# Kernel optimization log

Hardware: AMD Instinct MI355X
Metric: run time of the kernel (lower is better)

The kernel has to match this reference:

```python
import math
import jax, jax.numpy as jnp
import numpy as np

B, S, D, H = 1, 4096, 1024, 16
HD = D // H


def setup_inputs() -> dict:
    key = jax.random.key(0)
    ks = jax.random.split(key, 11)
    s = 0.02
    inp = {
        "q": jax.random.normal(ks[0], (B, S, D), jnp.float32),
        "k": jax.random.normal(ks[1], (B, S, D), jnp.float32),
        "v": jax.random.normal(ks[2], (B, S, D), jnp.float32),
        # causal boolean mask, broadcastable over [B, H, S, S]
        "mask": jnp.tril(jnp.ones((S, S), jnp.bool_))[None, None],
        "Wq": jax.random.normal(ks[3], (D, D), jnp.float32) * s,
        "bq": jnp.zeros((D,), jnp.float32),
        "Wk": jax.random.normal(ks[4], (D, D), jnp.float32) * s,
        "bk": jnp.zeros((D,), jnp.float32),
        "Wv": jax.random.normal(ks[5], (D, D), jnp.float32) * s,
        "bv": jnp.zeros((D,), jnp.float32),
        "Wo": jax.random.normal(ks[6], (D, D), jnp.float32) * s,
        "bo": jnp.zeros((D,), jnp.float32),
    }
    return inp


def reference(q, k, v, mask, Wq, bq, Wk, bk, Wv, bv, Wo, bo):
    # projections (torch Linear: x @ W.T + b; here W is stored already transposed)
    qp = (q @ Wq + bq).reshape(B, S, H, HD)
    kp = (k @ Wk + bk).reshape(B, S, H, HD)
    vp = (v @ Wv + bv).reshape(B, S, H, HD)
    # scores: [B, H, S, S]
    scores = jnp.einsum("bqhd,bkhd->bhqk", qp, kp) / math.sqrt(HD)
    scores = jnp.where(mask, scores, -jnp.inf)
    attn = jax.nn.softmax(scores, axis=-1)
    # context: [B, H, S, HD] -> [B, S, D]
    ctx = jnp.einsum("bhqk,bkhd->bqhd", attn, vp).reshape(B, S, D)
    return ctx @ Wo + bo
```

## Files before the change

### kernel.cpp

```cpp
#include <hip/hip_runtime.h>
#include <hip/hip_bf16.h>


#define S_LEN 4096
#define D_DIM 1024
#define NHEAD 16
#define HDIM  64

typedef __hip_bfloat16 bf16;
typedef __attribute__((ext_vector_type(8))) short bf16x8v;
typedef __attribute__((ext_vector_type(4))) float f32x4;

#define MFMA16(a, b, c) __builtin_amdgcn_mfma_f32_16x16x32_bf16((a), (b), (c), 0, 0, 0)

__device__ __forceinline__ void async_cp16(const void* g, void* l) {
    __builtin_amdgcn_global_load_lds(
        (const __attribute__((address_space(1))) unsigned int*)g,
        (__attribute__((address_space(3))) unsigned int*)l, 16, 0, 0);
}

__global__ __launch_bounds__(256) void cvt_bf16_k(
    const float* __restrict__ x0, const float* __restrict__ x1,
    const float* __restrict__ x2,
    bf16* __restrict__ y0, bf16* __restrict__ y1, bf16* __restrict__ y2)
{
    const float* x = (blockIdx.z == 0) ? x0 : (blockIdx.z == 1) ? x1 : x2;
    bf16*       y = (blockIdx.z == 0) ? y0 : (blockIdx.z == 1) ? y1 : y2;
    const size_t i = ((size_t)blockIdx.x * 256 + threadIdx.x);
    const float4 v = ((const float4*)x)[i];
    union { bf16 h[4]; short4 s; } u;
    u.h[0] = __float2bfloat16(v.x);
    u.h[1] = __float2bfloat16(v.y);
    u.h[2] = __float2bfloat16(v.z);
    u.h[3] = __float2bfloat16(v.w);
    ((short4*)y)[i] = u.s;
}

__global__ __launch_bounds__(256) void transpose_cvt_k(
    const float* __restrict__ W0, const float* __restrict__ W1,
    const float* __restrict__ W2, const float* __restrict__ W3,
    bf16* __restrict__ T0, bf16* __restrict__ T1,
    bf16* __restrict__ T2, bf16* __restrict__ T3)
{
    const float* W = (blockIdx.z == 0) ? W0 : (blockIdx.z == 1) ? W1
                   : (blockIdx.z == 2) ? W2 : W3;
    bf16*       Wt = (blockIdx.z == 0) ? T0 : (blockIdx.z == 1) ? T1
                   : (blockIdx.z == 2) ? T2 : T3;
    __shared__ float t[32][33];
    const int bx = blockIdx.x << 5, by = blockIdx.y << 5;
    const int tx = threadIdx.x & 31, ty = threadIdx.x >> 5;
#pragma unroll
    for (int i = 0; i < 32; i += 8)
        t[ty + i][tx] = W[(size_t)(by + ty + i) * D_DIM + bx + tx];
    __syncthreads();
#pragma unroll
    for (int i = 0; i < 32; i += 8)
        Wt[(size_t)(bx + ty + i) * D_DIM + by + tx] = __float2bfloat16(t[tx][ty + i]);
}

struct GemmJob {
    const bf16* A; const bf16* Wt; const float* bias; void* out;
    int mode; float scale;
};

__global__ __launch_bounds__(256) void gemm_k(GemmJob j0, GemmJob j1, GemmJob j2)
{
    const GemmJob j = (blockIdx.z == 0) ? j0 : (blockIdx.z == 1) ? j1 : j2;
    const int K = D_DIM;
    const int bn = blockIdx.x << 6;
    const int bm = blockIdx.y << 7;
    const int tid = threadIdx.x;
    const int w = tid >> 6, lane = tid & 63;
    const int col = lane & 15, g = lane >> 4;
    const int wr = (w >> 1) << 6, wc = (w & 1) << 5;

    __shared__ bf16 As[128 * 64];
    __shared__ bf16 Bs[64 * 64];

    f32x4 acc[4][2];
#pragma unroll
    for (int i = 0; i < 4; ++i)
#pragma unroll
        for (int jj = 0; jj < 2; ++jj) acc[i][jj] = (f32x4){0.f, 0.f, 0.f, 0.f};

    for (int kb = 0; kb < K; kb += 64) {
        __syncthreads();
#pragma unroll
        for (int e = 0; e < 4; ++e) {
            const int lin = (e << 8) + tid;
            const int row = lin >> 3, kc = lin & 7;
            async_cp16(j.A + (size_t)(bm + row) * K + kb + (kc << 3), &As[lin << 3]);
        }
#pragma unroll
        for (int e = 0; e < 2; ++e) {
            const int lin = (e << 8) + tid;
            const int row = lin >> 3, kc = lin & 7;
            async_cp16(j.Wt + (size_t)(bn + row) * K + kb + (kc << 3), &Bs[lin << 3]);
        }
        __syncthreads();

#pragma unroll
        for (int s = 0; s < 2; ++s) {
            bf16x8v af[4], bfv[2];
#pragma unroll
            for (int i = 0; i < 4; ++i)
                af[i] = *(const bf16x8v*)&As[((wr + (i << 4) + col) << 6) + (s << 5) + (g << 3)];
#pragma unroll
            for (int jj = 0; jj < 2; ++jj)
                bfv[jj] = *(const bf16x8v*)&Bs[((wc + (jj << 4) + col) << 6) + (s << 5) + (g << 3)];
#pragma unroll
            for (int i = 0; i < 4; ++i)
#pragma unroll
                for (int jj = 0; jj < 2; ++jj)
                    acc[i][jj] = MFMA16(af[i], bfv[jj], acc[i][jj]);
        }
    }

#pragma unroll
    for (int i = 0; i < 4; ++i)
#pragma unroll
    for (int jj = 0; jj < 2; ++jj)
#pragma unroll
    for (int reg = 0; reg < 4; ++reg) {
        const int row = bm + wr + (i << 4) + (g << 2) + reg;
        const int cg  = bn + wc + (jj << 4) + col;
        const float vv = (acc[i][jj][reg] + j.bias[cg]) * j.scale;
        if (j.mode == 0)
            ((bf16*)j.out)[(((size_t)(cg >> 6)) * S_LEN + row) * HDIM + (cg & 63)] =
                __float2bfloat16(vv);
        else if (j.mode == 2)
            ((bf16*)j.out)[((size_t)(cg >> 6) * HDIM + (cg & 63)) * S_LEN + row] =
                __float2bfloat16(vv);
        else
            ((float*)j.out)[(size_t)row * D_DIM + cg] = vv;
    }
}

__global__ __launch_bounds__(256) void attn_mfma_k(
    const bf16* __restrict__ Qp, const bf16* __restrict__ Kp,
    const bf16* __restrict__ Vt, bf16* __restrict__ ctx)
{
    __shared__ bf16 Ks[4096];
    __shared__ bf16 Vs[4096];
    __shared__ bf16 Ps[4][1024];

    const int bid = blockIdx.x;
    const int qb  = 63 - (bid >> 4);
    const int h   = bid & 15;
    const int q0  = qb << 6;
    const int tid = threadIdx.x, w = tid >> 6, lane = tid & 63;
    const int col = lane & 15, g = lane >> 4;

    const bf16* Kh = Kp + (size_t)h * S_LEN * HDIM;
    const bf16* Vh = Vt + (size_t)h * HDIM * S_LEN;

    const size_t qrow_base = ((size_t)h * S_LEN + q0 + (w << 4) + col) * HDIM + (g << 3);
    const bf16x8v qf0 = *(const bf16x8v*)(Qp + qrow_base);
    const bf16x8v qf1 = *(const bf16x8v*)(Qp + qrow_base + 32);

    const int sig_r = (col >> 2) | (((col & 3) ^ (g & 1)) << 2);
    const int pr0 = (((g) << 4) | sig_r) << 3;
    const int pr1 = (((4 + g) << 4) | sig_r) << 3;
    int pw[4][4];
#pragma unroll
    for (int t = 0; t < 4; ++t) {
        const int Gw = (t << 1) + (col >> 3);
#pragma unroll
        for (int reg = 0; reg < 4; ++reg) {
            const int sig = g | (((reg ^ (Gw & 1)) & 3) << 2);
            pw[t][reg] = (((Gw << 4) | sig) << 3) + (col & 7);
        }
    }

    float pl[4] = {0.f, 0.f, 0.f, 0.f};
    f32x4 acco[4];
#pragma unroll
    for (int t = 0; t < 4; ++t) acco[t] = (f32x4){0.f, 0.f, 0.f, 0.f};

    const int nkb = qb + 1;
    for (int kb = 0; kb < nkb; ++kb) {
        const int kk0 = kb << 6;
        __syncthreads();
#pragma unroll
        for (int e = 0; e < 2; ++e) {
            const int lin = (e << 8) + tid;
            const int t = lin >> 7, G = (lin >> 4) & 7, c = lin & 15;
            async_cp16(Kh + (size_t)(kk0 + (t << 4) + c) * HDIM + (G << 3),
                       &Ks[lin << 3]);
            async_cp16(Vh + (size_t)((t << 4) + c) * S_LEN + kk0 + (G << 3),
                       &Vs[lin << 3]);
        }
        __syncthreads();

        f32x4 sa[4];
#pragma unroll
        for (int t = 0; t < 4; ++t) sa[t] = (f32x4){0.f, 0.f, 0.f, 0.f};
#pragma unroll
        for (int t = 0; t < 4; ++t) {
            sa[t] = MFMA16(qf0, *(const bf16x8v*)&Ks[((t << 7) + (g << 4) + col) << 3], sa[t]);
            sa[t] = MFMA16(qf1, *(const bf16x8v*)&Ks[((t << 7) + 64 + (g << 4) + col) << 3], sa[t]);
        }

        const bool lastt = (kb == nkb - 1);
#pragma unroll
        for (int t = 0; t < 4; ++t) {
#pragma unroll
            for (int reg = 0; reg < 4; ++reg) {
                float p;
                if (lastt && (kk0 + (t << 4) + col > q0 + (w << 4) + (g << 2) + reg))
                    p = 0.f;
                else
                    p = __expf(sa[t][reg]);
                pl[reg] += p;
                Ps[w][pw[t][reg]] = __float2bfloat16(p);
            }
        }

        const bf16x8v pf0 = *(const bf16x8v*)&Ps[w][pr0];
        const bf16x8v pf1 = *(const bf16x8v*)&Ps[w][pr1];
#pragma unroll
        for (int t = 0; t < 4; ++t) {
            acco[t] = MFMA16(pf0, *(const bf16x8v*)&Vs[((t << 7) + (g << 4) + col) << 3], acco[t]);
            acco[t] = MFMA16(pf1, *(const bf16x8v*)&Vs[((t << 7) + 64 + (g << 4) + col) << 3], acco[t]);
        }
    }

    float lrow[4];
#pragma unroll
    for (int reg = 0; reg < 4; ++reg) {
        float l = pl[reg];
        l += __shfl_xor(l, 1);
        l += __shfl_xor(l, 2);
        l += __shfl_xor(l, 4);
        l += __shfl_xor(l, 8);
        lrow[reg] = l;
    }

#pragma unroll
    for (int t = 0; t < 4; ++t)
#pragma unroll
        for (int reg = 0; reg < 4; ++reg) {
            const int row = q0 + (w << 4) + (g << 2) + reg;
            ctx[(size_t)row * D_DIM + h * HDIM + (t << 4) + col] =
                __float2bfloat16(acco[t][reg] / lrow[reg]);
        }
}

extern "C" void kernel_launch(void* const* d_in, const int* in_sizes, int n_in,
                              void* d_out, int out_size, void* d_ws, size_t ws_size,
                              hipStream_t stream)
{
    const float* q  = (const float*)d_in[0];
    const float* k  = (const float*)d_in[1];
    const float* v  = (const float*)d_in[2];
    const float* Wq = (const float*)d_in[4];
    const float* bq = (const float*)d_in[5];
    const float* Wk = (const float*)d_in[6];
    const float* bk = (const float*)d_in[7];
    const float* Wv = (const float*)d_in[8];
    const float* bv = (const float*)d_in[9];
    const float* Wo = (const float*)d_in[10];
    const float* bo = (const float*)d_in[11];

    const size_t PE  = (size_t)S_LEN * D_DIM;
    const size_t WTE = (size_t)D_DIM * D_DIM;

    const dim3 tg(32, 32, 4);
    const dim3 gg(D_DIM / 64, S_LEN / 128, 1);
    const dim3 gg3(D_DIM / 64, S_LEN / 128, 3);
    const dim3 cg((unsigned)(PE / 1024), 1, 3);

    if (ws_size >= (size_t)64 * 1024 * 1024) {
        bf16* Qb = (bf16*)d_ws;
        bf16* Kb = Qb + PE;
        bf16* Vb = Kb + PE;
        bf16* Qp = Vb + PE;
        bf16* Kp = Qp + PE;
        bf16* Vt = Kp + PE;
        bf16* Wtq = Vt + PE;
        bf16* Wtk = Wtq + WTE;
        bf16* Wtv = Wtk + WTE;
        bf16* Wto = Wtv + WTE;
        bf16* ctx = Qb;

        transpose_cvt_k<<<tg, 256, 0, stream>>>(Wq, Wk, Wv, Wo, Wtq, Wtk, Wtv, Wto);
        cvt_bf16_k<<<cg, 256, 0, stream>>>(q, k, v, Qb, Kb, Vb);

        GemmJob jq{Qb, Wtq, bq, Qp, 0, 0.125f};
        GemmJob jk{Kb, Wtk, bk, Kp, 0, 1.0f};
        GemmJob jv{Vb, Wtv, bv, Vt, 2, 1.0f};
        gemm_k<<<gg3, 256, 0, stream>>>(jq, jk, jv);

        attn_mfma_k<<<dim3(1024), 256, 0, stream>>>(Qp, Kp, Vt, ctx);

        GemmJob jo{ctx, Wto, bo, d_out, 1, 1.0f};
        gemm_k<<<gg, 256, 0, stream>>>(jo, jo, jo);
    } else {
        bf16* X  = (bf16*)d_ws;
        bf16* Qp = X + PE;
        bf16* Kp = Qp + PE;
        bf16* Vt = Kp + PE;
        bf16* Wtq = Vt + PE;
        bf16* Wtk = Wtq + WTE;
        bf16* Wtv = Wtk + WTE;
        bf16* Wto = Wtv + WTE;

        transpose_cvt_k<<<tg, 256, 0, stream>>>(Wq, Wk, Wv, Wo, Wtq, Wtk, Wtv, Wto);

        const dim3 cg1((unsigned)(PE / 1024), 1, 1);
        cvt_bf16_k<<<cg1, 256, 0, stream>>>(q, q, q, X, X, X);
        GemmJob jq{X, Wtq, bq, Qp, 0, 0.125f};
        gemm_k<<<gg, 256, 0, stream>>>(jq, jq, jq);
        cvt_bf16_k<<<cg1, 256, 0, stream>>>(k, k, k, X, X, X);
        GemmJob jk{X, Wtk, bk, Kp, 0, 1.0f};
        gemm_k<<<gg, 256, 0, stream>>>(jk, jk, jk);
        cvt_bf16_k<<<cg1, 256, 0, stream>>>(v, v, v, X, X, X);
        GemmJob jv{X, Wtv, bv, Vt, 2, 1.0f};
        gemm_k<<<gg, 256, 0, stream>>>(jv, jv, jv);

        attn_mfma_k<<<dim3(1024), 256, 0, stream>>>(Qp, Kp, Vt, X);

        GemmJob jo{X, Wto, bo, d_out, 1, 1.0f};
        gemm_k<<<gg, 256, 0, stream>>>(jo, jo, jo);
    }
}
```

Before: 324.9 us.

## Double-buffer attention K/V tiles, use exp2 with folded log2e, widen GEMM tiles

The attention kernel now double-buffers its K/V shared-memory tiles, so the next block's async loads are issued before the current block is computed, and it keeps one barrier per iteration. The Q projection scale now includes log2(e), so softmax can call a native exp2 instead of __expf. The projection GEMMs move from 128x64 to 128x128 output tiles with 16 accumulators per wave, which improves operand reuse but halves the number of blocks and adds register and LDS pressure. The attention kernel's LDS use doubles, which may lower occupancy.

```diff
diff --git a/kernel.cpp b/kernel.cpp
--- a/kernel.cpp
+++ b/kernel.cpp
@@ -12,6 +12,14 @@
 typedef __attribute__((ext_vector_type(4))) float f32x4;
 
 #define MFMA16(a, b, c) __builtin_amdgcn_mfma_f32_16x16x32_bf16((a), (b), (c), 0, 0, 0)
+
+#if __has_builtin(__builtin_amdgcn_exp2f)
+#define EXP2F(x) __builtin_amdgcn_exp2f(x)
+#else
+#define EXP2F(x) exp2f(x)
+#endif
+
+#define QSCALE (0.125f * 1.4426950408889634f)
 
 __device__ __forceinline__ void async_cp16(const void* g, void* l) {
     __builtin_amdgcn_global_load_lds(
@@ -67,21 +75,21 @@
 {
     const GemmJob j = (blockIdx.z == 0) ? j0 : (blockIdx.z == 1) ? j1 : j2;
     const int K = D_DIM;
-    const int bn = blockIdx.x << 6;
+    const int bn = blockIdx.x << 7;
     const int bm = blockIdx.y << 7;
     const int tid = threadIdx.x;
     const int w = tid >> 6, lane = tid & 63;
     const int col = lane & 15, g = lane >> 4;
-    const int wr = (w >> 1) << 6, wc = (w & 1) << 5;
+    const int wr = (w >> 1) << 6, wc = (w & 1) << 6;
 
     __shared__ bf16 As[128 * 64];
-    __shared__ bf16 Bs[64 * 64];
-
-    f32x4 acc[4][2];
+    __shared__ bf16 Bs[128 * 64];
+
+    f32x4 acc[4][4];
 #pragma unroll
     for (int i = 0; i < 4; ++i)
 #pragma unroll
-        for (int jj = 0; jj < 2; ++jj) acc[i][jj] = (f32x4){0.f, 0.f, 0.f, 0.f};
+        for (int jj = 0; jj < 4; ++jj) acc[i][jj] = (f32x4){0.f, 0.f, 0.f, 0.f};
 
     for (int kb = 0; kb < K; kb += 64) {
         __syncthreads();
@@ -92,7 +100,7 @@
             async_cp16(j.A + (size_t)(bm + row) * K + kb + (kc << 3), &As[lin << 3]);
         }
 #pragma unroll
-        for (int e = 0; e < 2; ++e) {
+        for (int e = 0; e < 4; ++e) {
             const int lin = (e << 8) + tid;
             const int row = lin >> 3, kc = lin & 7;
             async_cp16(j.Wt + (size_t)(bn + row) * K + kb + (kc << 3), &Bs[lin << 3]);
@@ -101,17 +109,17 @@
 
 #pragma unroll
         for (int s = 0; s < 2; ++s) {
-            bf16x8v af[4], bfv[2];
+            bf16x8v af[4], bfv[4];
 #pragma unroll
             for (int i = 0; i < 4; ++i)
                 af[i] = *(const bf16x8v*)&As[((wr + (i << 4) + col) << 6) + (s << 5) + (g << 3)];
 #pragma unroll
-            for (int jj = 0; jj < 2; ++jj)
+            for (int jj = 0; jj < 4; ++jj)
                 bfv[jj] = *(const bf16x8v*)&Bs[((wc + (jj << 4) + col) << 6) + (s << 5) + (g << 3)];
 #pragma unroll
             for (int i = 0; i < 4; ++i)
 #pragma unroll
-                for (int jj = 0; jj < 2; ++jj)
+                for (int jj = 0; jj < 4; ++jj)
                     acc[i][jj] = MFMA16(af[i], bfv[jj], acc[i][jj]);
         }
     }
@@ -119,7 +127,7 @@
 #pragma unroll
     for (int i = 0; i < 4; ++i)
 #pragma unroll
-    for (int jj = 0; jj < 2; ++jj)
+    for (int jj = 0; jj < 4; ++jj)
 #pragma unroll
     for (int reg = 0; reg < 4; ++reg) {
         const int row = bm + wr + (i << 4) + (g << 2) + reg;
@@ -140,8 +148,8 @@
     const bf16* __restrict__ Qp, const bf16* __restrict__ Kp,
     const bf16* __restrict__ Vt, bf16* __restrict__ ctx)
 {
-    __shared__ bf16 Ks[4096];
-    __shared__ bf16 Vs[4096];
+    __shared__ bf16 Ks[2][4096];
+    __shared__ bf16 Vs[2][4096];
     __shared__ bf16 Ps[4][1024];
 
     const int bid = blockIdx.x;
@@ -178,27 +186,37 @@
     for (int t = 0; t < 4; ++t) acco[t] = (f32x4){0.f, 0.f, 0.f, 0.f};
 
     const int nkb = qb + 1;
-    for (int kb = 0; kb < nkb; ++kb) {
+
+    auto stage = [&](int buf, int kb) {
         const int kk0 = kb << 6;
-        __syncthreads();
 #pragma unroll
         for (int e = 0; e < 2; ++e) {
             const int lin = (e << 8) + tid;
             const int t = lin >> 7, G = (lin >> 4) & 7, c = lin & 15;
             async_cp16(Kh + (size_t)(kk0 + (t << 4) + c) * HDIM + (G << 3),
-                       &Ks[lin << 3]);
+                       &Ks[buf][lin << 3]);
             async_cp16(Vh + (size_t)((t << 4) + c) * S_LEN + kk0 + (G << 3),
-                       &Vs[lin << 3]);
-        }
-        __syncthreads();
+                       &Vs[buf][lin << 3]);
+        }
+    };
+
+    stage(0, 0);
+    __syncthreads();
+
+    for (int kb = 0; kb < nkb; ++kb) {
+        const int cur = kb & 1;
+        if (kb + 1 < nkb) stage(cur ^ 1, kb + 1);
+        const int kk0 = kb << 6;
+        const bf16* Kc = Ks[cur];
+        const bf16* Vc = Vs[cur];
 
         f32x4 sa[4];
 #pragma unroll
         for (int t = 0; t < 4; ++t) sa[t] = (f32x4){0.f, 0.f, 0.f, 0.f};
 #pragma unroll
         for (int t = 0; t < 4; ++t) {
-            sa[t] = MFMA16(qf0, *(const bf16x8v*)&Ks[((t << 7) + (g << 4) + col) << 3], sa[t]);
-            sa[t] = MFMA16(qf1, *(const bf16x8v*)&Ks[((t << 7) + 64 + (g << 4) + col) << 3], sa[t]);
+            sa[t] = MFMA16(qf0, *(const bf16x8v*)&Kc[((t << 7) + (g << 4) + col) << 3], sa[t]);
+            sa[t] = MFMA16(qf1, *(const bf16x8v*)&Kc[((t << 7) + 64 + (g << 4) + col) << 3], sa[t]);
         }
 
         const bool lastt = (kb == nkb - 1);
@@ -210,7 +228,7 @@
                 if (lastt && (kk0 + (t << 4) + col > q0 + (w << 4) + (g << 2) + reg))
                     p = 0.f;
                 else
-                    p = __expf(sa[t][reg]);
+                    p = EXP2F(sa[t][reg]);
                 pl[reg] += p;
                 Ps[w][pw[t][reg]] = __float2bfloat16(p);
             }
@@ -220,9 +238,11 @@
         const bf16x8v pf1 = *(const bf16x8v*)&Ps[w][pr1];
 #pragma unroll
         for (int t = 0; t < 4; ++t) {
-            acco[t] = MFMA16(pf0, *(const bf16x8v*)&Vs[((t << 7) + (g << 4) + col) << 3], acco[t]);
-            acco[t] = MFMA16(pf1, *(const bf16x8v*)&Vs[((t << 7) + 64 + (g << 4) + col) << 3], acco[t]);
-        }
+            acco[t] = MFMA16(pf0, *(const bf16x8v*)&Vc[((t << 7) + (g << 4) + col) << 3], acco[t]);
+            acco[t] = MFMA16(pf1, *(const bf16x8v*)&Vc[((t << 7) + 64 + (g << 4) + col) << 3], acco[t]);
+        }
+
+        __syncthreads();
     }
 
     float lrow[4];
@@ -266,8 +286,8 @@
     const size_t WTE = (size_t)D_DIM * D_DIM;
 
     const dim3 tg(32, 32, 4);
-    const dim3 gg(D_DIM / 64, S_LEN / 128, 1);
-    const dim3 gg3(D_DIM / 64, S_LEN / 128, 3);
+    const dim3 gg(D_DIM / 128, S_LEN / 128, 1);
+    const dim3 gg3(D_DIM / 128, S_LEN / 128, 3);
     const dim3 cg((unsigned)(PE / 1024), 1, 3);
 
     if (ws_size >= (size_t)64 * 1024 * 1024) {
@@ -286,7 +306,7 @@
         transpose_cvt_k<<<tg, 256, 0, stream>>>(Wq, Wk, Wv, Wo, Wtq, Wtk, Wtv, Wto);
         cvt_bf16_k<<<cg, 256, 0, stream>>>(q, k, v, Qb, Kb, Vb);
 
-        GemmJob jq{Qb, Wtq, bq, Qp, 0, 0.125f};
+        GemmJob jq{Qb, Wtq, bq, Qp, 0, QSCALE};
         GemmJob jk{Kb, Wtk, bk, Kp, 0, 1.0f};
         GemmJob jv{Vb, Wtv, bv, Vt, 2, 1.0f};
         gemm_k<<<gg3, 256, 0, stream>>>(jq, jk, jv);
@@ -309,7 +329,7 @@
 
         const dim3 cg1((unsigned)(PE / 1024), 1, 1);
         cvt_bf16_k<<<cg1, 256, 0, stream>>>(q, q, q, X, X, X);
-        GemmJob jq{X, Wtq, bq, Qp, 0, 0.125f};
+        GemmJob jq{X, Wtq, bq, Qp, 0, QSCALE};
         gemm_k<<<gg, 256, 0, stream>>>(jq, jq, jq);
         cvt_bf16_k<<<cg1, 256, 0, stream>>>(k, k, k, X, X, X);
         GemmJob jk{X, Wtk, bk, Kp, 0, 1.0f};
```

New measurement: 355.4 us. 9.4% more time.
